# Kernel optimization log

Hardware: AMD Instinct MI355X
Metric: run time of the kernel (lower is better)

## Reference

```python
import jax, jax.numpy as jnp
import numpy as np

H = 128        # hidden_size
K_DIFF = 32    # max_neighbors (opposite-type neighbors)
K = 64         # total neighbors per node (diff + same)
B = 4096       # batch of nodes
U = 100000     # num_users
I = 100000     # num_items


def setup_inputs() -> dict:
    key = jax.random.key(0)
    ks = jax.random.split(key, 20)
    rn = lambda k, shape, s=1.0: jax.random.normal(k, shape, dtype=jnp.float32) * s
    w = 0.05  # small init for weights/embeddings (xavier-ish)
    return {
        'user_text': rn(ks[0], (B, K + 1, H)),
        'item_text': rn(ks[1], (B, K + 1, H)),
        'user_diff_rel': rn(ks[2], (B, K_DIFF, H)),
        'item_diff_rel': rn(ks[3], (B, K_DIFF, H)),
        'user_inds': jax.random.randint(ks[4], (B, K + 1), 0, I),
        'item_inds': jax.random.randint(ks[5], (B, K + 1), 0, U),
        'user_emb': rn(ks[6], (U, H), w),
        'item_emb': rn(ks[7], (I, H), w),
        'ne_W1': rn(ks[8], (2 * H, H), w), 'ne_b1': jnp.zeros((H,), jnp.float32),
        'ne_W2': rn(ks[9], (H, H), w), 'ne_b2': jnp.zeros((H,), jnp.float32),
        'att_W1': rn(ks[10], (3 * H, H), w), 'att_b1': jnp.zeros((H,), jnp.float32),
        'att_W2': rn(ks[11], (H, 1), w), 'att_b2': jnp.zeros((1,), jnp.float32),
        'tr_W1': rn(ks[12], (2 * H, H), w), 'tr_b1': jnp.zeros((H,), jnp.float32),
        'tr_W2': rn(ks[13], (H, H), w), 'tr_b2': jnp.zeros((H,), jnp.float32),
    }


def _node_pref(text, inds, diff_rel, diff_tab, same_tab,
               ne_W1, ne_b1, ne_W2, ne_b2,
               att_W1, att_b1, att_W2, att_b2):
    # NodeEncoder: gather embeddings (first K_DIFF inds index opposite-type
    # table, the rest the same-type table), concat with semantic features, MLP.
    diff_emb = diff_tab[inds[:, :K_DIFF]]            # [B, Kd, H]
    same_emb = same_tab[inds[:, K_DIFF:]]            # [B, K-Kd+1, H]
    emb = jnp.concatenate([diff_emb, same_emb], axis=1)   # [B, K+1, H]
    x = jnp.concatenate([text, emb], axis=-1)             # [B, K+1, 2H]
    x = jax.nn.relu(x @ ne_W1 + ne_b1)
    nodes = jax.nn.relu(x @ ne_W2 + ne_b2)                # [B, K+1, H]

    this = nodes[:, -1]                                   # [B, H] (self node)
    ne = nodes[:, :-1]                                    # [B, K, H]
    same_rel = ne[:, K_DIFF:] * this[:, None, :]          # [B, K-Kd, H]
    rel = jnp.concatenate([diff_rel, same_rel], axis=1)   # [B, K, H]

    # Attention: concat(this, relation, neighbor) -> MLP -> softmax over neighbors
    feat = jnp.concatenate(
        [jnp.broadcast_to(this[:, None, :], ne.shape), rel, ne], axis=-1)  # [B,K,3H]
    h = jax.nn.relu(feat @ att_W1 + att_b1)
    s = jax.nn.relu(h @ att_W2 + att_b2)                  # [B, K, 1]
    att = jax.nn.softmax(s, axis=1)                       # softmax over neighbors
    agg = jnp.einsum('bko,bkh->bh', att, ne)              # weighted neighbor sum
    return jnp.concatenate([this, agg], axis=-1)          # [B, 2H]


def reference(user_text, item_text, user_diff_rel, item_diff_rel,
              user_inds, item_inds, user_emb, item_emb,
              ne_W1, ne_b1, ne_W2, ne_b2,
              att_W1, att_b1, att_W2, att_b2,
              tr_W1, tr_b1, tr_W2, tr_b2):
    u = _node_pref(user_text, user_inds, user_diff_rel, item_emb, user_emb,
                   ne_W1, ne_b1, ne_W2, ne_b2, att_W1, att_b1, att_W2, att_b2)
    it = _node_pref(item_text, item_inds, item_diff_rel, user_emb, item_emb,
                    ne_W1, ne_b1, ne_W2, ne_b2, att_W1, att_b1, att_W2, att_b2)
    transform = lambda x: jax.nn.relu(jax.nn.relu(x @ tr_W1 + tr_b1) @ tr_W2 + tr_b2)
    return (transform(u), transform(it))
```

## Files before the change

kernel.cpp:

```cpp
#include <hip/hip_runtime.h>
#include <cstdint>
#include <cstddef>

#define HH  128
#define KP1 65
#define KD  32
#define NB  4096


#define FM8(AS, W0, W1, ACCROW) do {                 \
    ACCROW[0] = fmaf(AS, W0.x, ACCROW[0]);           \
    ACCROW[1] = fmaf(AS, W0.y, ACCROW[1]);           \
    ACCROW[2] = fmaf(AS, W0.z, ACCROW[2]);           \
    ACCROW[3] = fmaf(AS, W0.w, ACCROW[3]);           \
    ACCROW[4] = fmaf(AS, W1.x, ACCROW[4]);           \
    ACCROW[5] = fmaf(AS, W1.y, ACCROW[5]);           \
    ACCROW[6] = fmaf(AS, W1.z, ACCROW[6]);           \
    ACCROW[7] = fmaf(AS, W1.w, ACCROW[7]);           \
} while (0)

__global__ __launch_bounds__(256, 2) void node_mlp_kernel(
    const float* __restrict__ user_text, const float* __restrict__ item_text,
    const int*   __restrict__ user_inds, const int*   __restrict__ item_inds,
    const float* __restrict__ user_emb,  const float* __restrict__ item_emb,
    const float* __restrict__ W1, const float* __restrict__ b1v,
    const float* __restrict__ W2, const float* __restrict__ b2v,
    float* __restrict__ nodes)
{
    __shared__ float a_ch[64][36];
    __shared__ float w_ch[32][128];
    __shared__ float x1s[64][132];

    const int tid  = threadIdx.x;
    const int trow = tid >> 4;
    const int tcol = tid & 15;
    const int c0   = tcol * 4;
    const int c1   = 64 + tcol * 4;
    const int row0 = blockIdx.x * 64;

    const int lr  = tid >> 2;
    const int seg = (tid & 3) * 8;
    const int gr_l   = row0 + lr;
    const int side_l = gr_l / (NB * KP1);
    const int rem_l  = gr_l - side_l * (NB * KP1);
    const int k_l    = rem_l % KP1;
    const float* text_row = (side_l ? item_text : user_text) + (size_t)rem_l * HH;
    const int    ind_l    = (side_l ? item_inds : user_inds)[rem_l];
    const float* tab_l    = (side_l == 0) ? ((k_l < KD) ? item_emb : user_emb)
                                          : ((k_l < KD) ? user_emb : item_emb);
    const float* emb_row  = tab_l + (size_t)ind_l * HH;

    const int wr = tid >> 3;
    const int ws = (tid & 7) * 16;

    float acc[4][8];
#pragma unroll
    for (int i = 0; i < 4; ++i)
#pragma unroll
        for (int j = 0; j < 8; ++j) acc[i][j] = 0.f;

    for (int kc = 0; kc < 2 * HH; kc += 32) {
        const float* asrc = (kc + seg < HH) ? (text_row + kc + seg)
                                            : (emb_row + (kc + seg - HH));
        float4 av0 = *(const float4*)(asrc);
        float4 av1 = *(const float4*)(asrc + 4);
        const float* wsrc = W1 + (size_t)(kc + wr) * HH + ws;
        float4 wv0 = *(const float4*)(wsrc);
        float4 wv1 = *(const float4*)(wsrc + 4);
        float4 wv2 = *(const float4*)(wsrc + 8);
        float4 wv3 = *(const float4*)(wsrc + 12);
        __syncthreads();
        *(float4*)&a_ch[lr][seg]      = av0;
        *(float4*)&a_ch[lr][seg + 4]  = av1;
        *(float4*)&w_ch[wr][ws]       = wv0;
        *(float4*)&w_ch[wr][ws + 4]   = wv1;
        *(float4*)&w_ch[wr][ws + 8]   = wv2;
        *(float4*)&w_ch[wr][ws + 12]  = wv3;
        __syncthreads();
#pragma unroll
        for (int kk4 = 0; kk4 < 8; ++kk4) {
            const int kb = kk4 * 4;
            float4 av[4];
#pragma unroll
            for (int i = 0; i < 4; ++i) av[i] = *(const float4*)&a_ch[trow * 4 + i][kb];
            float4 wA[4], wB[4];
#pragma unroll
            for (int t = 0; t < 4; ++t) {
                wA[t] = *(const float4*)&w_ch[kb + t][c0];
                wB[t] = *(const float4*)&w_ch[kb + t][c1];
            }
#pragma unroll
            for (int i = 0; i < 4; ++i) {
                FM8(av[i].x, wA[0], wB[0], acc[i]);
                FM8(av[i].y, wA[1], wB[1], acc[i]);
                FM8(av[i].z, wA[2], wB[2], acc[i]);
                FM8(av[i].w, wA[3], wB[3], acc[i]);
            }
        }
    }

    {
        float4 b0 = *(const float4*)(b1v + c0);
        float4 b1 = *(const float4*)(b1v + c1);
        const float bias[8] = {b0.x, b0.y, b0.z, b0.w, b1.x, b1.y, b1.z, b1.w};
#pragma unroll
        for (int i = 0; i < 4; ++i) {
            float tmp[8];
#pragma unroll
            for (int j = 0; j < 8; ++j) {
                tmp[j] = fmaxf(acc[i][j] + bias[j], 0.f);
                acc[i][j] = 0.f;
            }
            *(float4*)&x1s[trow * 4 + i][c0] = *(float4*)&tmp[0];
            *(float4*)&x1s[trow * 4 + i][c1] = *(float4*)&tmp[4];
        }
    }

    for (int kc = 0; kc < HH; kc += 32) {
        const float* wsrc = W2 + (size_t)(kc + wr) * HH + ws;
        float4 wv0 = *(const float4*)(wsrc);
        float4 wv1 = *(const float4*)(wsrc + 4);
        float4 wv2 = *(const float4*)(wsrc + 8);
        float4 wv3 = *(const float4*)(wsrc + 12);
        __syncthreads();
        *(float4*)&w_ch[wr][ws]      = wv0;
        *(float4*)&w_ch[wr][ws + 4]  = wv1;
        *(float4*)&w_ch[wr][ws + 8]  = wv2;
        *(float4*)&w_ch[wr][ws + 12] = wv3;
        __syncthreads();
#pragma unroll
        for (int kk4 = 0; kk4 < 8; ++kk4) {
            const int kb = kk4 * 4;
            float4 av[4];
#pragma unroll
            for (int i = 0; i < 4; ++i) av[i] = *(const float4*)&x1s[trow * 4 + i][kc + kb];
            float4 wA[4], wB[4];
#pragma unroll
            for (int t = 0; t < 4; ++t) {
                wA[t] = *(const float4*)&w_ch[kb + t][c0];
                wB[t] = *(const float4*)&w_ch[kb + t][c1];
            }
#pragma unroll
            for (int i = 0; i < 4; ++i) {
                FM8(av[i].x, wA[0], wB[0], acc[i]);
                FM8(av[i].y, wA[1], wB[1], acc[i]);
                FM8(av[i].z, wA[2], wB[2], acc[i]);
                FM8(av[i].w, wA[3], wB[3], acc[i]);
            }
        }
    }

    {
        float4 b0 = *(const float4*)(b2v + c0);
        float4 b1 = *(const float4*)(b2v + c1);
        const float bias[8] = {b0.x, b0.y, b0.z, b0.w, b1.x, b1.y, b1.z, b1.w};
#pragma unroll
        for (int i = 0; i < 4; ++i) {
            const int gr = row0 + trow * 4 + i;
            float tmp[8];
#pragma unroll
            for (int j = 0; j < 8; ++j) tmp[j] = fmaxf(acc[i][j] + bias[j], 0.f);
            float* dst = nodes + (size_t)gr * HH;
            *(float4*)(dst + c0) = *(float4*)&tmp[0];
            *(float4*)(dst + c1) = *(float4*)&tmp[4];
        }
    }
}

__global__ __launch_bounds__(256, 2) void att_kernel(
    const float* __restrict__ nodes,
    const float* __restrict__ user_diff_rel, const float* __restrict__ item_diff_rel,
    const float* __restrict__ A1, const float* __restrict__ ab1,
    const float* __restrict__ A2, const float* __restrict__ ab2,
    float* __restrict__ ufeat)
{
    __shared__ float ne_s[64][132];
    __shared__ float rel_s[32][132];
    __shared__ float w_ch[32][128];
    __shared__ float this_s[128];
    __shared__ float v0[128];
    __shared__ float att_s[64];

    const int tid  = threadIdx.x;
    const int bid  = blockIdx.x;
    const int side = bid >> 12;
    const int b    = bid & (NB - 1);

    const float* nbase = nodes + (size_t)((side * NB + b) * KP1) * HH;
    const float* drel  = (side ? item_diff_rel : user_diff_rel) + (size_t)b * KD * HH;

    if (tid < HH) this_s[tid] = nbase[64 * HH + tid];
    for (int idx = tid; idx < 64 * 32; idx += 256) {
        const int r = idx >> 5, c = (idx & 31) * 4;
        *(float4*)&ne_s[r][c] = *(const float4*)(nbase + r * HH + c);
    }
    for (int idx = tid; idx < 32 * 32; idx += 256) {
        const int r = idx >> 5, c = (idx & 31) * 4;
        *(float4*)&rel_s[r][c] = *(const float4*)(drel + r * HH + c);
    }
    __syncthreads();

    if (tid < HH) {
        float s = ab1[tid];
#pragma unroll 8
        for (int d = 0; d < HH; ++d) s = fmaf(this_s[d], A1[(size_t)d * HH + tid], s);
        v0[tid] = s;
    }
    __syncthreads();

    const int trow = tid >> 4;
    const int tcol = tid & 15;
    const int c0   = tcol * 4;
    const int c1   = 64 + tcol * 4;

    float acc[4][8];
    {
        float4 a0 = *(const float4*)&v0[c0];
        float4 a1 = *(const float4*)&v0[c1];
#pragma unroll
        for (int i = 0; i < 4; ++i) {
            acc[i][0] = a0.x; acc[i][1] = a0.y; acc[i][2] = a0.z; acc[i][3] = a0.w;
            acc[i][4] = a1.x; acc[i][5] = a1.y; acc[i][6] = a1.z; acc[i][7] = a1.w;
        }
    }

    const int wr = tid >> 3;
    const int ws = (tid & 7) * 16;

#pragma unroll
    for (int part = 0; part < 2; ++part) {
        const float* Wbase = A1 + (size_t)(HH + part * HH) * HH;
        for (int kc = 0; kc < HH; kc += 32) {
            const float* wsrc = Wbase + (size_t)(kc + wr) * HH + ws;
            float4 wv0 = *(const float4*)(wsrc);
            float4 wv1 = *(const float4*)(wsrc + 4);
            float4 wv2 = *(const float4*)(wsrc + 8);
            float4 wv3 = *(const float4*)(wsrc + 12);
            __syncthreads();
            *(float4*)&w_ch[wr][ws]      = wv0;
            *(float4*)&w_ch[wr][ws + 4]  = wv1;
            *(float4*)&w_ch[wr][ws + 8]  = wv2;
            *(float4*)&w_ch[wr][ws + 12] = wv3;
            __syncthreads();
#pragma unroll
            for (int kk4 = 0; kk4 < 8; ++kk4) {
                const int kb = kk4 * 4;
                const int d0 = kc + kb;
                float4 av[4];
                if (part == 0) {
                    float4 th4 = *(const float4*)&this_s[d0];
#pragma unroll
                    for (int i = 0; i < 4; ++i) {
                        const int r = trow * 4 + i;
                        if (r < KD) {
                            av[i] = *(const float4*)&rel_s[r][d0];
                        } else {
                            float4 n = *(const float4*)&ne_s[r][d0];
                            av[i].x = n.x * th4.x; av[i].y = n.y * th4.y;
                            av[i].z = n.z * th4.z; av[i].w = n.w * th4.w;
                        }
                    }
                } else {
#pragma unroll
                    for (int i = 0; i < 4; ++i)
                        av[i] = *(const float4*)&ne_s[trow * 4 + i][d0];
                }
                float4 wA[4], wB[4];
#pragma unroll
                for (int t = 0; t < 4; ++t) {
                    wA[t] = *(const float4*)&w_ch[kb + t][c0];
                    wB[t] = *(const float4*)&w_ch[kb + t][c1];
                }
#pragma unroll
                for (int i = 0; i < 4; ++i) {
                    FM8(av[i].x, wA[0], wB[0], acc[i]);
                    FM8(av[i].y, wA[1], wB[1], acc[i]);
                    FM8(av[i].z, wA[2], wB[2], acc[i]);
                    FM8(av[i].w, wA[3], wB[3], acc[i]);
                }
            }
        }
    }

    float w2v[8];
    {
        float4 a0 = *(const float4*)(A2 + c0);
        float4 a1 = *(const float4*)(A2 + c1);
        w2v[0] = a0.x; w2v[1] = a0.y; w2v[2] = a0.z; w2v[3] = a0.w;
        w2v[4] = a1.x; w2v[5] = a1.y; w2v[6] = a1.z; w2v[7] = a1.w;
    }
    const float bb2 = ab2[0];
    float p[4];
#pragma unroll
    for (int i = 0; i < 4; ++i) {
        p[i] = 0.f;
#pragma unroll
        for (int j = 0; j < 8; ++j) p[i] = fmaf(fmaxf(acc[i][j], 0.f), w2v[j], p[i]);
    }
#pragma unroll
    for (int m = 1; m < 16; m <<= 1)
#pragma unroll
        for (int i = 0; i < 4; ++i) p[i] += __shfl_xor(p[i], m);
    if (tcol == 0) {
#pragma unroll
        for (int i = 0; i < 4; ++i) att_s[trow * 4 + i] = fmaxf(p[i] + bb2, 0.f);
    }
    __syncthreads();

    if (tid < 64) {
        const float v = att_s[tid];
        float m = v;
#pragma unroll
        for (int off = 1; off < 64; off <<= 1) m = fmaxf(m, __shfl_xor(m, off));
        const float e = expf(v - m);
        float ssum = e;
#pragma unroll
        for (int off = 1; off < 64; off <<= 1) ssum += __shfl_xor(ssum, off);
        att_s[tid] = e / ssum;
    }
    __syncthreads();

    if (tid < HH) {
        float aggv = 0.f;
#pragma unroll
        for (int k = 0; k < 64; ++k) aggv = fmaf(att_s[k], ne_s[k][tid], aggv);
        float* orow = ufeat + (size_t)(side * NB + b) * 256;
        orow[tid]      = this_s[tid];
        orow[HH + tid] = aggv;
    }
}

__global__ __launch_bounds__(256, 2) void transform_kernel(
    const float* __restrict__ ufeat,
    const float* __restrict__ W1, const float* __restrict__ b1v,
    const float* __restrict__ W2, const float* __restrict__ b2v,
    float* __restrict__ out)
{
    __shared__ float a_ch[64][36];
    __shared__ float w_ch[32][128];
    __shared__ float x1s[64][132];

    const int tid  = threadIdx.x;
    const int trow = tid >> 4;
    const int tcol = tid & 15;
    const int c0   = tcol * 4;
    const int c1   = 64 + tcol * 4;
    const int row0 = blockIdx.x * 64;

    const int lr  = tid >> 2;
    const int seg = (tid & 3) * 8;
    const float* in_row = ufeat + (size_t)(row0 + lr) * 256;

    const int wr = tid >> 3;
    const int ws = (tid & 7) * 16;

    float acc[4][8];
#pragma unroll
    for (int i = 0; i < 4; ++i)
#pragma unroll
        for (int j = 0; j < 8; ++j) acc[i][j] = 0.f;

    for (int kc = 0; kc < 256; kc += 32) {
        float4 av0 = *(const float4*)(in_row + kc + seg);
        float4 av1 = *(const float4*)(in_row + kc + seg + 4);
        const float* wsrc = W1 + (size_t)(kc + wr) * HH + ws;
        float4 wv0 = *(const float4*)(wsrc);
        float4 wv1 = *(const float4*)(wsrc + 4);
        float4 wv2 = *(const float4*)(wsrc + 8);
        float4 wv3 = *(const float4*)(wsrc + 12);
        __syncthreads();
        *(float4*)&a_ch[lr][seg]     = av0;
        *(float4*)&a_ch[lr][seg + 4] = av1;
        *(float4*)&w_ch[wr][ws]      = wv0;
        *(float4*)&w_ch[wr][ws + 4]  = wv1;
        *(float4*)&w_ch[wr][ws + 8]  = wv2;
        *(float4*)&w_ch[wr][ws + 12] = wv3;
        __syncthreads();
#pragma unroll
        for (int kk4 = 0; kk4 < 8; ++kk4) {
            const int kb = kk4 * 4;
            float4 av[4];
#pragma unroll
            for (int i = 0; i < 4; ++i) av[i] = *(const float4*)&a_ch[trow * 4 + i][kb];
            float4 wA[4], wB[4];
#pragma unroll
            for (int t = 0; t < 4; ++t) {
                wA[t] = *(const float4*)&w_ch[kb + t][c0];
                wB[t] = *(const float4*)&w_ch[kb + t][c1];
            }
#pragma unroll
            for (int i = 0; i < 4; ++i) {
                FM8(av[i].x, wA[0], wB[0], acc[i]);
                FM8(av[i].y, wA[1], wB[1], acc[i]);
                FM8(av[i].z, wA[2], wB[2], acc[i]);
                FM8(av[i].w, wA[3], wB[3], acc[i]);
            }
        }
    }

    {
        float4 b0 = *(const float4*)(b1v + c0);
        float4 b1 = *(const float4*)(b1v + c1);
        const float bias[8] = {b0.x, b0.y, b0.z, b0.w, b1.x, b1.y, b1.z, b1.w};
#pragma unroll
        for (int i = 0; i < 4; ++i) {
            float tmp[8];
#pragma unroll
            for (int j = 0; j < 8; ++j) {
                tmp[j] = fmaxf(acc[i][j] + bias[j], 0.f);
                acc[i][j] = 0.f;
            }
            *(float4*)&x1s[trow * 4 + i][c0] = *(float4*)&tmp[0];
            *(float4*)&x1s[trow * 4 + i][c1] = *(float4*)&tmp[4];
        }
    }

    for (int kc = 0; kc < HH; kc += 32) {
        const float* wsrc = W2 + (size_t)(kc + wr) * HH + ws;
        float4 wv0 = *(const float4*)(wsrc);
        float4 wv1 = *(const float4*)(wsrc + 4);
        float4 wv2 = *(const float4*)(wsrc + 8);
        float4 wv3 = *(const float4*)(wsrc + 12);
        __syncthreads();
        *(float4*)&w_ch[wr][ws]      = wv0;
        *(float4*)&w_ch[wr][ws + 4]  = wv1;
        *(float4*)&w_ch[wr][ws + 8]  = wv2;
        *(float4*)&w_ch[wr][ws + 12] = wv3;
        __syncthreads();
#pragma unroll
        for (int kk4 = 0; kk4 < 8; ++kk4) {
            const int kb = kk4 * 4;
            float4 av[4];
#pragma unroll
            for (int i = 0; i < 4; ++i) av[i] = *(const float4*)&x1s[trow * 4 + i][kc + kb];
            float4 wA[4], wB[4];
#pragma unroll
            for (int t = 0; t < 4; ++t) {
                wA[t] = *(const float4*)&w_ch[kb + t][c0];
                wB[t] = *(const float4*)&w_ch[kb + t][c1];
            }
#pragma unroll
            for (int i = 0; i < 4; ++i) {
                FM8(av[i].x, wA[0], wB[0], acc[i]);
                FM8(av[i].y, wA[1], wB[1], acc[i]);
                FM8(av[i].z, wA[2], wB[2], acc[i]);
                FM8(av[i].w, wA[3], wB[3], acc[i]);
            }
        }
    }

    {
        float4 b0 = *(const float4*)(b2v + c0);
        float4 b1 = *(const float4*)(b2v + c1);
        const float bias[8] = {b0.x, b0.y, b0.z, b0.w, b1.x, b1.y, b1.z, b1.w};
#pragma unroll
        for (int i = 0; i < 4; ++i) {
            const int gr = row0 + trow * 4 + i;
            float tmp[8];
#pragma unroll
            for (int j = 0; j < 8; ++j) tmp[j] = fmaxf(acc[i][j] + bias[j], 0.f);
            float* dst = out + (size_t)gr * HH;
            *(float4*)(dst + c0) = *(float4*)&tmp[0];
            *(float4*)(dst + c1) = *(float4*)&tmp[4];
        }
    }
}

extern "C" void kernel_launch(void* const* d_in, const int* in_sizes, int n_in,
                              void* d_out, int out_size, void* d_ws, size_t ws_size,
                              hipStream_t stream)
{
    (void)in_sizes; (void)n_in; (void)out_size; (void)ws_size;

    const float* user_text     = (const float*)d_in[0];
    const float* item_text     = (const float*)d_in[1];
    const float* user_diff_rel = (const float*)d_in[2];
    const float* item_diff_rel = (const float*)d_in[3];
    const int*   user_inds     = (const int*)d_in[4];
    const int*   item_inds     = (const int*)d_in[5];
    const float* user_emb      = (const float*)d_in[6];
    const float* item_emb      = (const float*)d_in[7];
    const float* ne_W1         = (const float*)d_in[8];
    const float* ne_b1         = (const float*)d_in[9];
    const float* ne_W2         = (const float*)d_in[10];
    const float* ne_b2         = (const float*)d_in[11];
    const float* att_W1        = (const float*)d_in[12];
    const float* att_b1        = (const float*)d_in[13];
    const float* att_W2        = (const float*)d_in[14];
    const float* att_b2        = (const float*)d_in[15];
    const float* tr_W1         = (const float*)d_in[16];
    const float* tr_b1         = (const float*)d_in[17];
    const float* tr_W2         = (const float*)d_in[18];
    const float* tr_b2         = (const float*)d_in[19];

    float* nodes = (float*)d_ws;
    float* ufeat = nodes + (size_t)2 * NB * KP1 * HH;
    float* out   = (float*)d_out;

    const int rowsA = 2 * NB * KP1;
    hipLaunchKernelGGL(node_mlp_kernel, dim3(rowsA / 64), dim3(256), 0, stream,
                       user_text, item_text, user_inds, item_inds,
                       user_emb, item_emb, ne_W1, ne_b1, ne_W2, ne_b2, nodes);

    hipLaunchKernelGGL(att_kernel, dim3(2 * NB), dim3(256), 0, stream,
                       nodes, user_diff_rel, item_diff_rel,
                       att_W1, att_b1, att_W2, att_b2, ufeat);

    hipLaunchKernelGGL(transform_kernel, dim3(2 * NB / 64), dim3(256), 0, stream,
                       ufeat, tr_W1, tr_b1, tr_W2, tr_b2, out);
}
```

Baseline: 2.940 ms.

## Prefetch next weight/activation chunk into registers during compute in all GEMM kernels

Restructures the chunked GEMM loops in the node MLP, attention and transform kernels so the global loads for the next K-chunk are issued into registers before the current chunk's FMA loop, overlapping global latency with compute. The inner loop is rewritten to load weights per t-step, which reduces live registers. In the attention kernel the this·A1 projection is split across all 256 threads as two halves and merged into the accumulator init, and the two A1 parts are folded into one 8-chunk loop. The cost is extra register pressure from the in-flight prefetch buffers.

```diff
diff --git a/kernel.cpp b/kernel.cpp
--- a/kernel.cpp
+++ b/kernel.cpp
@@ -8,16 +8,41 @@
 #define NB  4096
 
 
-#define FM8(AS, W0, W1, ACCROW) do {                 \
-    ACCROW[0] = fmaf(AS, W0.x, ACCROW[0]);           \
-    ACCROW[1] = fmaf(AS, W0.y, ACCROW[1]);           \
-    ACCROW[2] = fmaf(AS, W0.z, ACCROW[2]);           \
-    ACCROW[3] = fmaf(AS, W0.w, ACCROW[3]);           \
-    ACCROW[4] = fmaf(AS, W1.x, ACCROW[4]);           \
-    ACCROW[5] = fmaf(AS, W1.y, ACCROW[5]);           \
-    ACCROW[6] = fmaf(AS, W1.z, ACCROW[6]);           \
-    ACCROW[7] = fmaf(AS, W1.w, ACCROW[7]);           \
+#define FMROW(AR, AS, W0, W1) do { \
+    AR[0] = fmaf(AS, W0.x, AR[0]); AR[1] = fmaf(AS, W0.y, AR[1]); \
+    AR[2] = fmaf(AS, W0.z, AR[2]); AR[3] = fmaf(AS, W0.w, AR[3]); \
+    AR[4] = fmaf(AS, W1.x, AR[4]); AR[5] = fmaf(AS, W1.y, AR[5]); \
+    AR[6] = fmaf(AS, W1.z, AR[6]); AR[7] = fmaf(AS, W1.w, AR[7]); } while (0)
+
+#define DO_CHUNK(R0, R1, R2, R3) do {                                   \
+    _Pragma("unroll")                                                   \
+    for (int kk4 = 0; kk4 < 8; ++kk4) {                                 \
+        const int kb = kk4 * 4;                                         \
+        float a0v[4], a1v[4], a2v[4], a3v[4];                           \
+        *(float4*)a0v = *(const float4*)((R0) + kb);                    \
+        *(float4*)a1v = *(const float4*)((R1) + kb);                    \
+        *(float4*)a2v = *(const float4*)((R2) + kb);                    \
+        *(float4*)a3v = *(const float4*)((R3) + kb);                    \
+        _Pragma("unroll")                                               \
+        for (int t = 0; t < 4; ++t) {                                   \
+            float4 wAv = *(const float4*)&w_ch[kb + t][c0];             \
+            float4 wBv = *(const float4*)&w_ch[kb + t][c1];             \
+            FMROW(acc[0], a0v[t], wAv, wBv);                            \
+            FMROW(acc[1], a1v[t], wAv, wBv);                            \
+            FMROW(acc[2], a2v[t], wAv, wBv);                            \
+            FMROW(acc[3], a3v[t], wAv, wBv);                            \
+        }                                                               \
+    }                                                                   \
 } while (0)
+
+#define LOADW(WPTR, KC) do {                                            \
+    const float* wsrc = (WPTR) + (size_t)((KC) + wr) * HH + ws;         \
+    wv0 = *(const float4*)(wsrc);      wv1 = *(const float4*)(wsrc + 4);\
+    wv2 = *(const float4*)(wsrc + 8);  wv3 = *(const float4*)(wsrc + 12); } while (0)
+
+#define STOREW() do {                                                   \
+    *(float4*)&w_ch[wr][ws]      = wv0; *(float4*)&w_ch[wr][ws + 4]  = wv1; \
+    *(float4*)&w_ch[wr][ws + 8]  = wv2; *(float4*)&w_ch[wr][ws + 12] = wv3; } while (0)
 
 __global__ __launch_bounds__(256, 2) void node_mlp_kernel(
     const float* __restrict__ user_text, const float* __restrict__ item_text,
@@ -53,50 +78,34 @@
     const int wr = tid >> 3;
     const int ws = (tid & 7) * 16;
 
+#define LOADA1(KC) do {                                                  \
+    const float* asrc = ((KC) + seg < HH) ? (text_row + (KC) + seg)      \
+                                          : (emb_row + ((KC) + seg - HH));\
+    av0 = *(const float4*)(asrc); av1 = *(const float4*)(asrc + 4); } while (0)
+
     float acc[4][8];
 #pragma unroll
     for (int i = 0; i < 4; ++i)
 #pragma unroll
         for (int j = 0; j < 8; ++j) acc[i][j] = 0.f;
 
+    float4 av0, av1, wv0, wv1, wv2, wv3;
+    LOADA1(0); LOADW(W1, 0);
+
+    const float* ar0 = &a_ch[trow * 4 + 0][0];
+    const float* ar1 = &a_ch[trow * 4 + 1][0];
+    const float* ar2 = &a_ch[trow * 4 + 2][0];
+    const float* ar3 = &a_ch[trow * 4 + 3][0];
+
     for (int kc = 0; kc < 2 * HH; kc += 32) {
-        const float* asrc = (kc + seg < HH) ? (text_row + kc + seg)
-                                            : (emb_row + (kc + seg - HH));
-        float4 av0 = *(const float4*)(asrc);
-        float4 av1 = *(const float4*)(asrc + 4);
-        const float* wsrc = W1 + (size_t)(kc + wr) * HH + ws;
-        float4 wv0 = *(const float4*)(wsrc);
-        float4 wv1 = *(const float4*)(wsrc + 4);
-        float4 wv2 = *(const float4*)(wsrc + 8);
-        float4 wv3 = *(const float4*)(wsrc + 12);
-        __syncthreads();
-        *(float4*)&a_ch[lr][seg]      = av0;
-        *(float4*)&a_ch[lr][seg + 4]  = av1;
-        *(float4*)&w_ch[wr][ws]       = wv0;
-        *(float4*)&w_ch[wr][ws + 4]   = wv1;
-        *(float4*)&w_ch[wr][ws + 8]   = wv2;
-        *(float4*)&w_ch[wr][ws + 12]  = wv3;
-        __syncthreads();
-#pragma unroll
-        for (int kk4 = 0; kk4 < 8; ++kk4) {
-            const int kb = kk4 * 4;
-            float4 av[4];
-#pragma unroll
-            for (int i = 0; i < 4; ++i) av[i] = *(const float4*)&a_ch[trow * 4 + i][kb];
-            float4 wA[4], wB[4];
-#pragma unroll
-            for (int t = 0; t < 4; ++t) {
-                wA[t] = *(const float4*)&w_ch[kb + t][c0];
-                wB[t] = *(const float4*)&w_ch[kb + t][c1];
-            }
-#pragma unroll
-            for (int i = 0; i < 4; ++i) {
-                FM8(av[i].x, wA[0], wB[0], acc[i]);
-                FM8(av[i].y, wA[1], wB[1], acc[i]);
-                FM8(av[i].z, wA[2], wB[2], acc[i]);
-                FM8(av[i].w, wA[3], wB[3], acc[i]);
-            }
-        }
+        __syncthreads();
+        *(float4*)&a_ch[lr][seg]     = av0;
+        *(float4*)&a_ch[lr][seg + 4] = av1;
+        STOREW();
+        __syncthreads();
+        if (kc + 32 < 2 * HH) { LOADA1(kc + 32); LOADW(W1, kc + 32); }
+        else                  { LOADW(W2, 0); }
+        DO_CHUNK(ar0, ar1, ar2, ar3);
     }
 
     {
@@ -117,37 +126,15 @@
     }
 
     for (int kc = 0; kc < HH; kc += 32) {
-        const float* wsrc = W2 + (size_t)(kc + wr) * HH + ws;
-        float4 wv0 = *(const float4*)(wsrc);
-        float4 wv1 = *(const float4*)(wsrc + 4);
-        float4 wv2 = *(const float4*)(wsrc + 8);
-        float4 wv3 = *(const float4*)(wsrc + 12);
-        __syncthreads();
-        *(float4*)&w_ch[wr][ws]      = wv0;
-        *(float4*)&w_ch[wr][ws + 4]  = wv1;
-        *(float4*)&w_ch[wr][ws + 8]  = wv2;
-        *(float4*)&w_ch[wr][ws + 12] = wv3;
-        __syncthreads();
-#pragma unroll
-        for (int kk4 = 0; kk4 < 8; ++kk4) {
-            const int kb = kk4 * 4;
-            float4 av[4];
-#pragma unroll
-            for (int i = 0; i < 4; ++i) av[i] = *(const float4*)&x1s[trow * 4 + i][kc + kb];
-            float4 wA[4], wB[4];
-#pragma unroll
-            for (int t = 0; t < 4; ++t) {
-                wA[t] = *(const float4*)&w_ch[kb + t][c0];
-                wB[t] = *(const float4*)&w_ch[kb + t][c1];
-            }
-#pragma unroll
-            for (int i = 0; i < 4; ++i) {
-                FM8(av[i].x, wA[0], wB[0], acc[i]);
-                FM8(av[i].y, wA[1], wB[1], acc[i]);
-                FM8(av[i].z, wA[2], wB[2], acc[i]);
-                FM8(av[i].w, wA[3], wB[3], acc[i]);
-            }
-        }
+        __syncthreads();
+        STOREW();
+        __syncthreads();
+        if (kc + 32 < HH) LOADW(W2, kc + 32);
+        const float* xr0 = &x1s[trow * 4 + 0][kc];
+        const float* xr1 = &x1s[trow * 4 + 1][kc];
+        const float* xr2 = &x1s[trow * 4 + 2][kc];
+        const float* xr3 = &x1s[trow * 4 + 3][kc];
+        DO_CHUNK(xr0, xr1, xr2, xr3);
     }
 
     {
@@ -165,6 +152,7 @@
             *(float4*)(dst + c1) = *(float4*)&tmp[4];
         }
     }
+#undef LOADA1
 }
 
 __global__ __launch_bounds__(256, 2) void att_kernel(
@@ -178,7 +166,7 @@
     __shared__ float rel_s[32][132];
     __shared__ float w_ch[32][128];
     __shared__ float this_s[128];
-    __shared__ float v0[128];
+    __shared__ float v0p[2][128];
     __shared__ float att_s[64];
 
     const int tid  = threadIdx.x;
@@ -189,6 +177,13 @@
     const float* nbase = nodes + (size_t)((side * NB + b) * KP1) * HH;
     const float* drel  = (side ? item_diff_rel : user_diff_rel) + (size_t)b * KD * HH;
 
+    const int trow = tid >> 4;
+    const int tcol = tid & 15;
+    const int c0   = tcol * 4;
+    const int c1   = 64 + tcol * 4;
+    const int wr   = tid >> 3;
+    const int ws   = (tid & 7) * 16;
+
     if (tid < HH) this_s[tid] = nbase[64 * HH + tid];
     for (int idx = tid; idx < 64 * 32; idx += 256) {
         const int r = idx >> 5, c = (idx & 31) * 4;
@@ -198,86 +193,77 @@
         const int r = idx >> 5, c = (idx & 31) * 4;
         *(float4*)&rel_s[r][c] = *(const float4*)(drel + r * HH + c);
     }
+
+    float4 wv0, wv1, wv2, wv3;
+    LOADW(A1 + (size_t)HH * HH, 0);
     __syncthreads();
 
-    if (tid < HH) {
-        float s = ab1[tid];
+    {
+        const int vcol  = tid & 127;
+        const int vhalf = tid >> 7;
+        float s = 0.f;
+        const float* ap = A1 + (size_t)(vhalf * 64) * HH + vcol;
 #pragma unroll 8
-        for (int d = 0; d < HH; ++d) s = fmaf(this_s[d], A1[(size_t)d * HH + tid], s);
-        v0[tid] = s;
-    }
-    __syncthreads();
-
-    const int trow = tid >> 4;
-    const int tcol = tid & 15;
-    const int c0   = tcol * 4;
-    const int c1   = 64 + tcol * 4;
+        for (int d = 0; d < 64; ++d)
+            s = fmaf(this_s[vhalf * 64 + d], ap[(size_t)d * HH], s);
+        v0p[vhalf][vcol] = s;
+    }
 
     float acc[4][8];
-    {
-        float4 a0 = *(const float4*)&v0[c0];
-        float4 a1 = *(const float4*)&v0[c1];
-#pragma unroll
-        for (int i = 0; i < 4; ++i) {
-            acc[i][0] = a0.x; acc[i][1] = a0.y; acc[i][2] = a0.z; acc[i][3] = a0.w;
-            acc[i][4] = a1.x; acc[i][5] = a1.y; acc[i][6] = a1.z; acc[i][7] = a1.w;
-        }
-    }
-
-    const int wr = tid >> 3;
-    const int ws = (tid & 7) * 16;
-
-#pragma unroll
-    for (int part = 0; part < 2; ++part) {
-        const float* Wbase = A1 + (size_t)(HH + part * HH) * HH;
-        for (int kc = 0; kc < HH; kc += 32) {
-            const float* wsrc = Wbase + (size_t)(kc + wr) * HH + ws;
-            float4 wv0 = *(const float4*)(wsrc);
-            float4 wv1 = *(const float4*)(wsrc + 4);
-            float4 wv2 = *(const float4*)(wsrc + 8);
-            float4 wv3 = *(const float4*)(wsrc + 12);
-            __syncthreads();
-            *(float4*)&w_ch[wr][ws]      = wv0;
-            *(float4*)&w_ch[wr][ws + 4]  = wv1;
-            *(float4*)&w_ch[wr][ws + 8]  = wv2;
-            *(float4*)&w_ch[wr][ws + 12] = wv3;
-            __syncthreads();
-#pragma unroll
-            for (int kk4 = 0; kk4 < 8; ++kk4) {
-                const int kb = kk4 * 4;
-                const int d0 = kc + kb;
-                float4 av[4];
-                if (part == 0) {
-                    float4 th4 = *(const float4*)&this_s[d0];
-#pragma unroll
-                    for (int i = 0; i < 4; ++i) {
-                        const int r = trow * 4 + i;
-                        if (r < KD) {
-                            av[i] = *(const float4*)&rel_s[r][d0];
-                        } else {
-                            float4 n = *(const float4*)&ne_s[r][d0];
-                            av[i].x = n.x * th4.x; av[i].y = n.y * th4.y;
-                            av[i].z = n.z * th4.z; av[i].w = n.w * th4.w;
-                        }
-                    }
-                } else {
-#pragma unroll
-                    for (int i = 0; i < 4; ++i)
-                        av[i] = *(const float4*)&ne_s[trow * 4 + i][d0];
+    const float* relbase = &rel_s[trow * 4][0];
+    const float* nebase  = &ne_s[trow * 4][0];
+
+    for (int cc = 0; cc < 8; ++cc) {
+        __syncthreads();
+        STOREW();
+        __syncthreads();
+        if (cc < 7) LOADW(A1 + (size_t)(HH + (cc + 1) * 32) * HH, 0);
+        if (cc == 0) {
+            float4 p0A = *(const float4*)&v0p[0][c0];
+            float4 p0B = *(const float4*)&v0p[0][c1];
+            float4 p1A = *(const float4*)&v0p[1][c0];
+            float4 p1B = *(const float4*)&v0p[1][c1];
+            float4 bA  = *(const float4*)(ab1 + c0);
+            float4 bB  = *(const float4*)(ab1 + c1);
+            const float base8[8] = {
+                p0A.x + p1A.x + bA.x, p0A.y + p1A.y + bA.y,
+                p0A.z + p1A.z + bA.z, p0A.w + p1A.w + bA.w,
+                p0B.x + p1B.x + bB.x, p0B.y + p1B.y + bB.y,
+                p0B.z + p1B.z + bB.z, p0B.w + p1B.w + bB.w };
+#pragma unroll
+            for (int i = 0; i < 4; ++i)
+#pragma unroll
+                for (int j = 0; j < 8; ++j) acc[i][j] = base8[j];
+        }
+        const int  kcp  = (cc & 3) * 32;
+        const bool isP0 = (cc < 4);
+        const float* base = (isP0 && trow < 8) ? (relbase + kcp) : (nebase + kcp);
+        const bool mulThis = isP0 && (trow >= 8);
+#pragma unroll
+        for (int kk4 = 0; kk4 < 8; ++kk4) {
+            const int kb = kk4 * 4;
+            float a0v[4], a1v[4], a2v[4], a3v[4];
+            *(float4*)a0v = *(const float4*)(base + 0 * 132 + kb);
+            *(float4*)a1v = *(const float4*)(base + 1 * 132 + kb);
+            *(float4*)a2v = *(const float4*)(base + 2 * 132 + kb);
+            *(float4*)a3v = *(const float4*)(base + 3 * 132 + kb);
+            if (mulThis) {
+                float th[4];
+                *(float4*)th = *(const float4*)&this_s[kcp + kb];
+#pragma unroll
+                for (int t = 0; t < 4; ++t) {
+                    a0v[t] *= th[t]; a1v[t] *= th[t];
+                    a2v[t] *= th[t]; a3v[t] *= th[t];
                 }
-                float4 wA[4], wB[4];
-#pragma unroll
-                for (int t = 0; t < 4; ++t) {
-                    wA[t] = *(const float4*)&w_ch[kb + t][c0];
-                    wB[t] = *(const float4*)&w_ch[kb + t][c1];
-                }
-#pragma unroll
-                for (int i = 0; i < 4; ++i) {
-                    FM8(av[i].x, wA[0], wB[0], acc[i]);
-                    FM8(av[i].y, wA[1], wB[1], acc[i]);
-                    FM8(av[i].z, wA[2], wB[2], acc[i]);
-                    FM8(av[i].w, wA[3], wB[3], acc[i]);
-                }
+            }
+#pragma unroll
+            for (int t = 0; t < 4; ++t) {
+                float4 wAv = *(const float4*)&w_ch[kb + t][c0];
+                float4 wBv = *(const float4*)&w_ch[kb + t][c1];
+                FMROW(acc[0], a0v[t], wAv, wBv);
+                FMROW(acc[1], a1v[t], wAv, wBv);
+                FMROW(acc[2], a2v[t], wAv, wBv);
+                FMROW(acc[3], a3v[t], wAv, wBv);
             }
         }
     }
@@ -360,42 +346,30 @@
 #pragma unroll
         for (int j = 0; j < 8; ++j) acc[i][j] = 0.f;
 
+    float4 av0, av1, wv0, wv1, wv2, wv3;
+    av0 = *(const float4*)(in_row + seg);
+    av1 = *(const float4*)(in_row + seg + 4);
+    LOADW(W1, 0);
+
+    const float* ar0 = &a_ch[trow * 4 + 0][0];
+    const float* ar1 = &a_ch[trow * 4 + 1][0];
+    const float* ar2 = &a_ch[trow * 4 + 2][0];
+    const float* ar3 = &a_ch[trow * 4 + 3][0];
+
     for (int kc = 0; kc < 256; kc += 32) {
-        float4 av0 = *(const float4*)(in_row + kc + seg);
-        float4 av1 = *(const float4*)(in_row + kc + seg + 4);
-        const float* wsrc = W1 + (size_t)(kc + wr) * HH + ws;
-        float4 wv0 = *(const float4*)(wsrc);
-        float4 wv1 = *(const float4*)(wsrc + 4);
-        float4 wv2 = *(const float4*)(wsrc + 8);
-        float4 wv3 = *(const float4*)(wsrc + 12);
         __syncthreads();
         *(float4*)&a_ch[lr][seg]     = av0;
         *(float4*)&a_ch[lr][seg + 4] = av1;
-        *(float4*)&w_ch[wr][ws]      = wv0;
-        *(float4*)&w_ch[wr][ws + 4]  = wv1;
-        *(float4*)&w_ch[wr][ws + 8]  = wv2;
-        *(float4*)&w_ch[wr][ws + 12] = wv3;
-        __syncthreads();
-#pragma unroll
-        for (int kk4 = 0; kk4 < 8; ++kk4) {
-            const int kb = kk4 * 4;
-            float4 av[4];
-#pragma unroll
-            for (int i = 0; i < 4; ++i) av[i] = *(const float4*)&a_ch[trow * 4 + i][kb];
-            float4 wA[4], wB[4];
-#pragma unroll
-            for (int t = 0; t < 4; ++t) {
-                wA[t] = *(const float4*)&w_ch[kb + t][c0];
-                wB[t] = *(const float4*)&w_ch[kb + t][c1];
-            }
-#pragma unroll
-            for (int i = 0; i < 4; ++i) {
-                FM8(av[i].x, wA[0], wB[0], acc[i]);
-                FM8(av[i].y, wA[1], wB[1], acc[i]);
-                FM8(av[i].z, wA[2], wB[2], acc[i]);
-                FM8(av[i].w, wA[3], wB[3], acc[i]);
-            }
-        }
+        STOREW();
+        __syncthreads();
+        if (kc + 32 < 256) {
+            av0 = *(const float4*)(in_row + kc + 32 + seg);
+            av1 = *(const float4*)(in_row + kc + 32 + seg + 4);
+            LOADW(W1, kc + 32);
+        } else {
+            LOADW(W2, 0);
+        }
+        DO_CHUNK(ar0, ar1, ar2, ar3);
     }
 
     {
@@ -416,37 +390,15 @@
     }
 
     for (int kc = 0; kc < HH; kc += 32) {
-        const float* wsrc = W2 + (size_t)(kc + wr) * HH + ws;
-        float4 wv0 = *(const float4*)(wsrc);
-        float4 wv1 = *(const float4*)(wsrc + 4);
-        float4 wv2 = *(const float4*)(wsrc + 8);
-        float4 wv3 = *(const float4*)(wsrc + 12);
-        __syncthreads();
-        *(float4*)&w_ch[wr][ws]      = wv0;
-        *(float4*)&w_ch[wr][ws + 4]  = wv1;
-        *(float4*)&w_ch[wr][ws + 8]  = wv2;
-        *(float4*)&w_ch[wr][ws + 12] = wv3;
-        __syncthreads();
-#pragma unroll
-        for (int kk4 = 0; kk4 < 8; ++kk4) {
-            const int kb = kk4 * 4;
-            float4 av[4];
-#pragma unroll
-            for (int i = 0; i < 4; ++i) av[i] = *(const float4*)&x1s[trow * 4 + i][kc + kb];
-            float4 wA[4], wB[4];
-#pragma unroll
-            for (int t = 0; t < 4; ++t) {
-                wA[t] = *(const float4*)&w_ch[kb + t][c0];
-                wB[t] = *(const float4*)&w_ch[kb + t][c1];
-            }
-#pragma unroll
-            for (int i = 0; i < 4; ++i) {
-                FM8(av[i].x, wA[0], wB[0], acc[i]);
-                FM8(av[i].y, wA[1], wB[1], acc[i]);
-                FM8(av[i].z, wA[2], wB[2], acc[i]);
-                FM8(av[i].w, wA[3], wB[3], acc[i]);
-            }
-        }
+        __syncthreads();
+        STOREW();
+        __syncthreads();
+        if (kc + 32 < HH) LOADW(W2, kc + 32);
+        const float* xr0 = &x1s[trow * 4 + 0][kc];
+        const float* xr1 = &x1s[trow * 4 + 1][kc];
+        const float* xr2 = &x1s[trow * 4 + 2][kc];
+        const float* xr3 = &x1s[trow * 4 + 3][kc];
+        DO_CHUNK(xr0, xr1, xr2, xr3);
     }
 
     {
```

New measurement: 4.578 ms. 55.7% more time.
